# Kernel optimization log

Measured on AMD Instinct MI355X. Metric: run time of the kernel, lower is better.

The kernel has to match this reference:

```python
import jax, jax.numpy as jnp
import numpy as np

N_HEAD = 32
N_KV_HEAD = 8
HEAD_DIM = 64
ROPE_THETA = 10000.0


def apply_rope(x):
    # x: [B, H, T, D], interleaved-pair RoPE (rotary_embedding_torch style)
    B, H, T, D = x.shape
    inv_freq = 1.0 / (ROPE_THETA ** (jnp.arange(0, D, 2, dtype=jnp.float32) / D))  # [D/2]
    ang = jnp.arange(T, dtype=jnp.float32)[:, None] * inv_freq[None, :]  # [T, D/2]
    cos = jnp.cos(ang)[None, None].astype(x.dtype)  # [1,1,T,D/2]
    sin = jnp.sin(ang)[None, None].astype(x.dtype)
    xe = x[..., 0::2]
    xo = x[..., 1::2]
    re = xe * cos - xo * sin
    ro = xo * cos + xe * sin
    return jnp.stack([re, ro], axis=-1).reshape(B, H, T, D)


def setup_inputs() -> dict:
    key = jax.random.key(0)
    ks = jax.random.split(key, 5)
    B, T, C = 2, 2048, 2048
    kv_dim = N_KV_HEAD * HEAD_DIM
    s = 0.02
    return {
        "x": jax.random.normal(ks[0], (B, T, C), jnp.float32),
        "wq": jax.random.normal(ks[1], (C, C), jnp.float32) * s,
        "wk": jax.random.normal(ks[2], (C, kv_dim), jnp.float32) * s,
        "wv": jax.random.normal(ks[3], (C, kv_dim), jnp.float32) * s,
        "wo": jax.random.normal(ks[4], (C, C), jnp.float32) * s,
    }


def reference(x, wq, wk, wv, wo):
    B, T, C = x.shape
    hd = HEAD_DIM
    q = (x @ wq).reshape(B, T, N_HEAD, hd).transpose(0, 2, 1, 3)      # [B,H,T,d]
    k = (x @ wk).reshape(B, T, N_KV_HEAD, hd).transpose(0, 2, 1, 3)   # [B,Hkv,T,d]
    v = (x @ wv).reshape(B, T, N_KV_HEAD, hd).transpose(0, 2, 1, 3)
    q = apply_rope(q)
    k = apply_rope(k)
    rep = N_HEAD // N_KV_HEAD
    k = jnp.repeat(k, rep, axis=1)  # repeat_interleave over head dim
    v = jnp.repeat(v, rep, axis=1)
    att = jnp.einsum('bhqd,bhkd->bhqk', q, k) * (1.0 / np.sqrt(hd))
    causal = jnp.tril(jnp.ones((T, T), dtype=bool))
    att = jnp.where(causal[None, None], att, jnp.finfo(att.dtype).min)
    att = jax.nn.softmax(att, axis=-1)
    y = jnp.einsum('bhqk,bhkd->bhqd', att, v)
    y = y.transpose(0, 2, 1, 3).reshape(B, T, C)
    return y @ wo
```

## Files before the change

### kernel.cpp

```cpp
#include <hip/hip_runtime.h>
#include <hip/hip_bf16.h>
#include <cstdint>
#include <cstddef>


using bf16 = __hip_bfloat16;
using f32x4  = __attribute__((ext_vector_type(4))) float;
using f32x16 = __attribute__((ext_vector_type(16))) float;
using short8 = __attribute__((ext_vector_type(8))) short;
using u32x4  = __attribute__((ext_vector_type(4))) unsigned int;

typedef __attribute__((address_space(1))) const void* gp1_t;
typedef __attribute__((address_space(3))) void*       lp3_t;

#define GLOAD_LDS16(g, l)                                                     \
  __builtin_amdgcn_global_load_lds((gp1_t)(const void*)(g), (lp3_t)(void*)(l), 16, 0, 0)

#define MFMA32(a, b, c) __builtin_amdgcn_mfma_f32_32x32x16_bf16(a, b, c, 0, 0, 0)

static constexpr int Bd  = 2;
static constexpr int Td  = 2048;
static constexpr int Cd  = 2048;
static constexpr int NH  = 32;
static constexpr int NKV = 8;
static constexpr int HD  = 64;
static constexpr int Md  = Bd * Td;

__device__ inline float bf2f(unsigned short u) {
  union { unsigned int i; float f; } v; v.i = ((unsigned int)u) << 16; return v.f;
}
__device__ inline unsigned short f2bfbits(float f) {
  union { float f; unsigned int u; } v; v.f = f;
  unsigned int r = v.u + 0x7fffu + ((v.u >> 16) & 1u);
  return (unsigned short)(r >> 16);
}
__device__ inline unsigned int pkbf(float a, float b) {
  unsigned int r;
  asm("v_cvt_pk_bf16_f32 %0, %1, %2" : "=v"(r) : "v"(a), "v"(b));
  return r;
}
__device__ inline void plswapf(float& a, float& b) {
  asm("v_permlane32_swap_b32 %0, %1" : "+v"(a), "+v"(b));
}
__device__ inline void plswapu(unsigned int& a, unsigned int& b) {
  asm("v_permlane32_swap_b32 %0, %1" : "+v"(a), "+v"(b));
}
__device__ inline float hmax16(const f32x16& v) {
  float a0 = fmaxf(v[0], v[1]),   a1 = fmaxf(v[2], v[3]);
  float a2 = fmaxf(v[4], v[5]),   a3 = fmaxf(v[6], v[7]);
  float a4 = fmaxf(v[8], v[9]),   a5 = fmaxf(v[10], v[11]);
  float a6 = fmaxf(v[12], v[13]), a7 = fmaxf(v[14], v[15]);
  float b0 = fmaxf(a0, a1), b1 = fmaxf(a2, a3);
  float b2 = fmaxf(a4, a5), b3 = fmaxf(a6, a7);
  return fmaxf(fmaxf(b0, b1), fmaxf(b2, b3));
}
__device__ inline float hsum16(const f32x16& v) {
  float a0 = v[0]+v[1],   a1 = v[2]+v[3],   a2 = v[4]+v[5],   a3 = v[6]+v[7];
  float a4 = v[8]+v[9],   a5 = v[10]+v[11], a6 = v[12]+v[13], a7 = v[14]+v[15];
  float b0 = a0+a1, b1 = a2+a3, b2 = a4+a5, b3 = a6+a7;
  return (b0+b1)+(b2+b3);
}

__global__ __launch_bounds__(256) void prep1_kernel(const float* __restrict__ x,
                                                    const float* __restrict__ wq,
                                                    const float* __restrict__ wk,
                                                    const float* __restrict__ wv,
                                                    bf16* __restrict__ xb,
                                                    bf16* __restrict__ w1) {
  __shared__ float tile[32][33];
  int bid = blockIdx.x, tid = threadIdx.x;
  if (bid < 8192) {
    int i = bid * 256 + tid;
    float4 v = ((const float4*)x)[i];
    ushort4 o;
    o.x = f2bfbits(v.x); o.y = f2bfbits(v.y); o.z = f2bfbits(v.z); o.w = f2bfbits(v.w);
    ((ushort4*)xb)[i] = o;
    return;
  }
  const float* in; bf16* out; int Cc, bx, by;
  if (bid < 12288)      { int l = bid - 8192;  in = wq; out = w1;                        Cc = 2048; bx = l & 63; by = l >> 6; }
  else if (bid < 13312) { int l = bid - 12288; in = wk; out = w1 + (size_t)2048 * 2048;  Cc = 512;  bx = l & 15; by = l >> 4; }
  else                  { int l = bid - 13312; in = wv; out = w1 + (size_t)2560 * 2048;  Cc = 512;  bx = l & 15; by = l >> 4; }
  int tx = tid & 31, ty = tid >> 5;
  int col = bx * 32 + tx;
#pragma unroll
  for (int i = 0; i < 4; ++i) {
    int row = by * 32 + ty + i * 8;
    tile[ty + i * 8][tx] = in[(size_t)row * Cc + col];
  }
  __syncthreads();
#pragma unroll
  for (int i = 0; i < 4; ++i) {
    int orow = bx * 32 + ty + i * 8;
    int ocol = by * 32 + tx;
    out[(size_t)orow * 2048 + ocol] = __float2bfloat16(tile[tx][ty + i * 8]);
  }
}

__global__ __launch_bounds__(256) void transpose_f2b(const float* __restrict__ in,
                                                     bf16* __restrict__ out,
                                                     int R, int Cc) {
  __shared__ float tile[32][33];
  int tx = threadIdx.x & 31, ty = threadIdx.x >> 5;
  int bx = blockIdx.x, by = blockIdx.y;
  int col = bx * 32 + tx;
#pragma unroll
  for (int i = 0; i < 4; ++i) {
    int row = by * 32 + ty + i * 8;
    tile[ty + i * 8][tx] = in[(size_t)row * Cc + col];
  }
  __syncthreads();
#pragma unroll
  for (int i = 0; i < 4; ++i) {
    int orow = bx * 32 + ty + i * 8;
    int ocol = by * 32 + tx;
    out[(size_t)orow * R + ocol] = __float2bfloat16(tile[tx][ty + i * 8]);
  }
}

template <int MODE>
__global__ __launch_bounds__(256, 2) void gemm_bf16(const bf16* __restrict__ A,
                                                    const bf16* __restrict__ Bt,
                                                    void* __restrict__ Cp,
                                                    int M, int N, int K) {
  __shared__ __align__(16) bf16 Al[2][128 * 64];
  __shared__ __align__(16) bf16 Bl[2][128 * 64];
  int tid = threadIdx.x;
  int w = tid >> 6, lane = tid & 63;
  int lr = lane & 15, lg = lane >> 4;
  int m0 = blockIdx.x * 128, n0 = blockIdx.y * 128;
  int wr = w >> 1, wc = w & 1;
  f32x4 acc[4][4] = {};

  size_t Kb = (size_t)K * 2;
  int c8 = lane & 7, r8 = lane >> 3;
  const char* Asrc = (const char*)A + (size_t)(m0 + w * 8 + r8) * Kb + ((c8 ^ r8) << 4);
  const char* Bsrc = (const char*)Bt + (size_t)(n0 + w * 8 + r8) * Kb + ((c8 ^ r8) << 4);

#define GSTAGE(kt, bb) do {                                                   \
    char* ald = (char*)&Al[bb][0] + w * 1024;                                 \
    char* bld = (char*)&Bl[bb][0] + w * 1024;                                 \
    _Pragma("unroll")                                                         \
    for (int j = 0; j < 4; ++j) {                                             \
      GLOAD_LDS16(Asrc + (size_t)j * 32 * Kb + (size_t)(kt) * 2, ald + j * 4096); \
      GLOAD_LDS16(Bsrc + (size_t)j * 32 * Kb + (size_t)(kt) * 2, bld + j * 4096); \
    }                                                                         \
  } while (0)

  int nkt = K >> 6;
  GSTAGE(0, 0);
  __syncthreads();

  for (int t = 0; t < nkt; ++t) {
    int cur = t & 1;
    if (t + 1 < nkt) GSTAGE((t + 1) << 6, cur ^ 1);
    const char* Ab = (const char*)&Al[cur][0];
    const char* Bb = (const char*)&Bl[cur][0];
#pragma unroll
    for (int kk = 0; kk < 2; ++kk) {
      short8 af[4], bfr[4];
#pragma unroll
      for (int f = 0; f < 4; ++f) {
        int ra = wr * 64 + f * 16 + lr;
        int rb = wc * 64 + f * 16 + lr;
        int cb = (((kk << 2) | lg) ^ (lr & 7)) << 4;
        af[f]  = *(const short8*)(Ab + (size_t)ra * 128 + cb);
        bfr[f] = *(const short8*)(Bb + (size_t)rb * 128 + cb);
      }
#pragma unroll
      for (int i = 0; i < 4; ++i)
#pragma unroll
        for (int j = 0; j < 4; ++j)
          acc[i][j] = __builtin_amdgcn_mfma_f32_16x16x32_bf16(af[i], bfr[j], acc[i][j], 0, 0, 0);
    }
    __syncthreads();
  }
#undef GSTAGE

  bf16* Qb  = (bf16*)Cp;
  bf16* Kb2 = Qb + (size_t)Bd * NH * Td * HD;
  bf16* Vtb = Kb2 + (size_t)Bd * NKV * Td * HD;

  if (MODE == 3 && n0 >= 2560) {
    int h  = (n0 - 2560 + wc * 64) >> 6;
    int b  = m0 >> 11;
    int tg = (m0 & 2047) + wr * 64;
    char* tb = (w < 2 ? (char*)&Al[0][0] : (char*)&Bl[0][0]) + (w & 1) * 8192;
#pragma unroll
    for (int i = 0; i < 4; ++i)
#pragma unroll
      for (int j = 0; j < 4; ++j)
#pragma unroll
        for (int r = 0; r < 4; r += 2) {
          int d  = j * 16 + lr;
          int tt = i * 16 + lg * 4 + r;
          unsigned int pk = pkbf(acc[i][j][r], acc[i][j][r + 1]);
          *(unsigned int*)(tb + (((size_t)d * 128 + tt * 2) ^ ((d & 7) << 4))) = pk;
        }
    asm volatile("s_waitcnt lgkmcnt(0)" ::: "memory");
    __builtin_amdgcn_sched_barrier(0);
    char* Vdst = (char*)Vtb + ((((size_t)b * NKV + h) * 64) * Td + tg) * 2;
#pragma unroll
    for (int p = 0; p < 8; ++p) {
      int d  = p * 8 + (lane >> 3);
      int tc = lane & 7;
      u32x4 v = *(const u32x4*)(tb + (((size_t)d * 128 + tc * 16) ^ ((d & 7) << 4)));
      *(u32x4*)(Vdst + (size_t)d * Td * 2 + tc * 16) = v;
    }
    return;
  }

  if (MODE == 3) {
    const float RC = -0.41524101186092029f;
    float sc = (n0 < 2048) ? 0.18033688011112042f : 1.0f;
    int odd = lane & 1;
#pragma unroll
    for (int j = 0; j < 4; ++j) {
      int ncol = n0 + wc * 64 + j * 16 + lr;
      int d  = ncol & 63;
      float inv = __builtin_amdgcn_exp2f((float)(d >> 1) * RC);
#pragma unroll
      for (int i = 0; i < 4; ++i) {
#pragma unroll
        for (int r = 0; r < 4; ++r) {
          int mrow = m0 + wr * 64 + i * 16 + lg * 4 + r;
          int t = mrow & 2047;
          float v = acc[i][j][r];
          float p = __shfl_xor(v, 1);
          float rev = (float)t * inv * 0.15915494309189535f;
          rev = rev - floorf(rev);
          float s = __builtin_amdgcn_sinf(rev);
          float c = __builtin_amdgcn_cosf(rev);
          float res = odd ? (v * c + p * s) : (v * c - p * s);
          res *= sc;
          int b = mrow >> 11;
          if (n0 < 2048) {
            int h = ncol >> 6;
            Qb[(((size_t)b * NH + h) * Td + t) * HD + d] = __float2bfloat16(res);
          } else {
            int h = (ncol - 2048) >> 6;
            Kb2[(((size_t)b * NKV + h) * Td + t) * HD + d] = __float2bfloat16(res);
          }
        }
      }
    }
    return;
  }

#pragma unroll
  for (int i = 0; i < 4; ++i)
#pragma unroll
    for (int j = 0; j < 4; ++j)
#pragma unroll
      for (int r = 0; r < 4; ++r) {
        int mrow = m0 + wr * 64 + i * 16 + lg * 4 + r;
        int ncol = n0 + wc * 64 + j * 16 + lr;
        ((float*)Cp)[(size_t)mrow * N + ncol] = acc[i][j][r];
      }
}

__global__ __launch_bounds__(512, 4) void attn_kernel(const bf16* __restrict__ Q,
                                                      const bf16* __restrict__ K,
                                                      const bf16* __restrict__ Vt,
                                                      bf16* __restrict__ Y) {
  __shared__ __align__(16) char lds[2 * 16384];
  int tid = threadIdx.x, w = tid >> 6, lane = tid & 63;
  int lq = lane & 31;
  int H  = lane >> 5;
  int qb = 7 - (int)blockIdx.y;
  int bh = blockIdx.x;
  int b = bh >> 5, h = bh & 31, kvh = h >> 2;
  int q0w = qb * 256 + w * 32;
  int qg  = q0w + lq;
  int tmax = qb * 4 + (w >> 1);
  int Nt   = qb * 4 + 4;

  const bf16* Qp = Q + (((size_t)b * NH + h) * Td) * HD;
  const char* Kg = (const char*)(K + (((size_t)b * NKV + kvh) * Td) * HD);
  const char* Vg = (const char*)(Vt + (((size_t)b * NKV + kvh) * HD) * Td);

  short8 qf[4];
#pragma unroll
  for (int ck = 0; ck < 4; ++ck)
    qf[ck] = *(const short8*)(Qp + (size_t)qg * HD + ck * 16 + H * 8);

  int srow   = lane >> 3;
  int scol16 = ((lane & 7) ^ srow) << 4;
  const char* Ksrc0 = Kg + (size_t)(w * 8 + srow) * 128 + scol16;
  const char* Vsrc0 = Vg + (size_t)(w * 8 + srow) * 4096 + scol16;
  char* KldsW[2] = { lds + w * 1024,          lds + 16384 + w * 1024 };
  char* VldsW[2] = { lds + 8192 + w * 1024,   lds + 24576 + w * 1024 };

#define STAGE_KV(tt, bb) do {                                                 \
    GLOAD_LDS16(Ksrc0 + (size_t)(tt) * 64 * 128, KldsW[bb]);                  \
    GLOAD_LDS16(Vsrc0 + (size_t)(tt) * 128,      VldsW[bb]);                  \
  } while (0)

  f32x16 acc0 = {}, acc1 = {};
  float m = -3e38f, l = 0.0f;
  int swz = (lq & 7) << 4;
  int rb0 = lq * 128, rb1 = (32 + lq) * 128;

  STAGE_KV(0, 0);
  asm volatile("s_waitcnt vmcnt(0)" ::: "memory");
  __syncthreads();

  for (int t = 0; t < Nt; ++t) {
    int cur = t & 1;
    if (t + 1 < Nt) STAGE_KV(t + 1, cur ^ 1);
    if (t <= tmax) {
      const char* Kl = lds + cur * 16384;
      const char* Vl = Kl + 8192;
      f32x16 s0 = {}, s1 = {};
      __builtin_amdgcn_s_setprio(1);
#pragma unroll
      for (int ck = 0; ck < 4; ++ck) {
        int c = (H * 16 + ck * 32) ^ swz;
        short8 kf0 = *(const short8*)(Kl + rb0 + c);
        short8 kf1 = *(const short8*)(Kl + rb1 + c);
        s0 = MFMA32(kf0, qf[ck], s0);
        s1 = MFMA32(kf1, qf[ck], s1);
      }
      __builtin_amdgcn_s_setprio(0);
      if (t == tmax) {
        int kvb = t * 64;
#pragma unroll
        for (int rr = 0; rr < 16; ++rr) {
          int krel = (rr & 3) + 8 * (rr >> 2) + 4 * H;
          if (kvb + krel > qg)      s0[rr] = -3e38f;
          if (kvb + 32 + krel > qg) s1[rr] = -3e38f;
        }
      }
      float mx = fmaxf(hmax16(s0), hmax16(s1));
      {
        float mb = mx;
        asm("" : "+v"(mb));
        plswapf(mx, mb);
        mx = fmaxf(mx, mb);
      }
      if (__any(mx > m + 8.0f)) {
        float mn = fmaxf(m, mx);
        float al = __builtin_amdgcn_exp2f(m - mn);
        m = mn;
        l *= al;
#pragma unroll
        for (int rr = 0; rr < 16; ++rr) { acc0[rr] *= al; acc1[rr] *= al; }
      }
#pragma unroll
      for (int rr = 0; rr < 16; ++rr) {
        s0[rr] = __builtin_amdgcn_exp2f(s0[rr] - m);
        s1[rr] = __builtin_amdgcn_exp2f(s1[rr] - m);
      }
      float ps = hsum16(s0) + hsum16(s1);
      {
        float pb = ps;
        asm("" : "+v"(pb));
        plswapf(ps, pb);
        ps += pb;
      }
      l += ps;
      short8 pf[4];
#pragma unroll
      for (int tt = 0; tt < 2; ++tt) {
        const f32x16& sv = tt ? s1 : s0;
#pragma unroll
        for (int a2 = 0; a2 < 2; ++a2) {
          unsigned int A0 = pkbf(sv[8*a2 + 0], sv[8*a2 + 1]);
          unsigned int A1 = pkbf(sv[8*a2 + 2], sv[8*a2 + 3]);
          unsigned int B0 = pkbf(sv[8*a2 + 4], sv[8*a2 + 5]);
          unsigned int B1 = pkbf(sv[8*a2 + 6], sv[8*a2 + 7]);
          plswapu(A0, B0);
          plswapu(A1, B1);
          u32x4 t4;
          t4[0] = A0; t4[1] = A1; t4[2] = B0; t4[3] = B1;
          pf[2*tt + a2] = __builtin_bit_cast(short8, t4);
        }
      }
      __builtin_amdgcn_s_setprio(1);
#pragma unroll
      for (int ks = 0; ks < 4; ++ks) {
        int c = (H * 16 + ks * 32) ^ swz;
        short8 vf0 = *(const short8*)(Vl + rb0 + c);
        short8 vf1 = *(const short8*)(Vl + rb1 + c);
        acc0 = MFMA32(vf0, pf[ks], acc0);
        acc1 = MFMA32(vf1, pf[ks], acc1);
      }
      __builtin_amdgcn_s_setprio(0);
    }
    asm volatile("s_waitcnt vmcnt(0)" ::: "memory");
    __syncthreads();
  }
#undef STAGE_KV

  float rn = 1.0f / l;
  bf16* Yp = Y + ((size_t)b * Td + qg) * Cd + h * HD;
#pragma unroll
  for (int rr = 0; rr < 16; rr += 2) {
    int d = (rr & 3) + 8 * (rr >> 2) + 4 * H;
    unsigned int w0 = pkbf(acc0[rr] * rn, acc0[rr + 1] * rn);
    unsigned int w1 = pkbf(acc1[rr] * rn, acc1[rr + 1] * rn);
    *(unsigned int*)(Yp + d)      = w0;
    *(unsigned int*)(Yp + 32 + d) = w1;
  }
}

extern "C" void kernel_launch(void* const* d_in, const int* in_sizes, int n_in,
                              void* d_out, int out_size, void* d_ws, size_t ws_size,
                              hipStream_t stream) {
  const float* x  = (const float*)d_in[0];
  const float* wq = (const float*)d_in[1];
  const float* wk = (const float*)d_in[2];
  const float* wv = (const float*)d_in[3];
  const float* wo = (const float*)d_in[4];

  char* ws = (char*)d_ws;
  const size_t o_xb = 0;
  const size_t o_w1 = o_xb + (size_t)Md * Cd * 2;
  const size_t o_Q  = o_w1 + (size_t)3072 * Cd * 2;
  const size_t o_K  = o_Q + (size_t)Bd * NH * Td * HD * 2;
  const size_t o_V  = o_K + (size_t)Bd * NKV * Td * HD * 2;

  bf16* xb  = (bf16*)(ws + o_xb);
  bf16* w1  = (bf16*)(ws + o_w1);
  bf16* Qb  = (bf16*)(ws + o_Q);
  bf16* Kb  = (bf16*)(ws + o_K);
  bf16* Vtb = (bf16*)(ws + o_V);
  bf16* yb  = xb;

  prep1_kernel<<<dim3(14336), dim3(256), 0, stream>>>(x, wq, wk, wv, xb, w1);
  gemm_bf16<3><<<dim3(Md / 128, 3072 / 128), dim3(256), 0, stream>>>(xb, w1, Qb, Md, 3072, Cd);
  transpose_f2b<<<dim3(Cd / 32, Cd / 32), dim3(256), 0, stream>>>(wo, w1, Cd, Cd);
  attn_kernel<<<dim3(Bd * NH, 8), dim3(512), 0, stream>>>(Qb, Kb, Vtb, yb);
  gemm_bf16<2><<<dim3(Md / 128, Cd / 128), dim3(256), 0, stream>>>(yb, w1, d_out, Md, Cd, Cd);
}
```

Measured before the change: 198.3 us.

## Use two waves per GEMM block with 64x128 per-wave tiles

Restructures the bf16 GEMM from four waves each owning a 64x64 sub-tile to two waves each owning 64 rows by the full 128 columns. This doubles accumulators per wave and raises register-level reuse of B fragments, cutting LDS reads per MFMA. It also rewrites staging, the V-transpose epilogue and the RoPE epilogue for the new layout. The trade-off is fewer waves per block for latency hiding and more register pressure, which may lower occupancy.

```diff
diff --git a/kernel.cpp b/kernel.cpp
--- a/kernel.cpp
+++ b/kernel.cpp
@@ -119,7 +119,7 @@
 }
 
 template <int MODE>
-__global__ __launch_bounds__(256, 2) void gemm_bf16(const bf16* __restrict__ A,
+__global__ __launch_bounds__(128, 2) void gemm_bf16(const bf16* __restrict__ A,
                                                     const bf16* __restrict__ Bt,
                                                     void* __restrict__ Cp,
                                                     int M, int N, int K) {
@@ -129,21 +129,20 @@
   int w = tid >> 6, lane = tid & 63;
   int lr = lane & 15, lg = lane >> 4;
   int m0 = blockIdx.x * 128, n0 = blockIdx.y * 128;
-  int wr = w >> 1, wc = w & 1;
-  f32x4 acc[4][4] = {};
+  f32x4 acc[4][8] = {};
 
   size_t Kb = (size_t)K * 2;
   int c8 = lane & 7, r8 = lane >> 3;
-  const char* Asrc = (const char*)A + (size_t)(m0 + w * 8 + r8) * Kb + ((c8 ^ r8) << 4);
-  const char* Bsrc = (const char*)Bt + (size_t)(n0 + w * 8 + r8) * Kb + ((c8 ^ r8) << 4);
+  const char* Asrc = (const char*)A + (size_t)(m0 + w * 64 + r8) * Kb + ((c8 ^ r8) << 4);
+  const char* Bsrc = (const char*)Bt + (size_t)(n0 + w * 64 + r8) * Kb + ((c8 ^ r8) << 4);
 
 #define GSTAGE(kt, bb) do {                                                   \
-    char* ald = (char*)&Al[bb][0] + w * 1024;                                 \
-    char* bld = (char*)&Bl[bb][0] + w * 1024;                                 \
+    char* ald = (char*)&Al[bb][0] + w * 8192;                                 \
+    char* bld = (char*)&Bl[bb][0] + w * 8192;                                 \
     _Pragma("unroll")                                                         \
-    for (int j = 0; j < 4; ++j) {                                             \
-      GLOAD_LDS16(Asrc + (size_t)j * 32 * Kb + (size_t)(kt) * 2, ald + j * 4096); \
-      GLOAD_LDS16(Bsrc + (size_t)j * 32 * Kb + (size_t)(kt) * 2, bld + j * 4096); \
+    for (int j = 0; j < 8; ++j) {                                             \
+      GLOAD_LDS16(Asrc + (size_t)j * 8 * Kb + (size_t)(kt) * 2, ald + j * 1024); \
+      GLOAD_LDS16(Bsrc + (size_t)j * 8 * Kb + (size_t)(kt) * 2, bld + j * 1024); \
     }                                                                         \
   } while (0)
 
@@ -158,19 +157,18 @@
     const char* Bb = (const char*)&Bl[cur][0];
 #pragma unroll
     for (int kk = 0; kk < 2; ++kk) {
-      short8 af[4], bfr[4];
-#pragma unroll
-      for (int f = 0; f < 4; ++f) {
-        int ra = wr * 64 + f * 16 + lr;
-        int rb = wc * 64 + f * 16 + lr;
-        int cb = (((kk << 2) | lg) ^ (lr & 7)) << 4;
-        af[f]  = *(const short8*)(Ab + (size_t)ra * 128 + cb);
-        bfr[f] = *(const short8*)(Bb + (size_t)rb * 128 + cb);
-      }
+      int cb = (((kk << 2) | lg) ^ (lr & 7)) << 4;
+      short8 af[4], bfr[8];
+#pragma unroll
+      for (int f = 0; f < 4; ++f)
+        af[f] = *(const short8*)(Ab + (size_t)(w * 64 + f * 16 + lr) * 128 + cb);
+#pragma unroll
+      for (int j = 0; j < 8; ++j)
+        bfr[j] = *(const short8*)(Bb + (size_t)(j * 16 + lr) * 128 + cb);
 #pragma unroll
       for (int i = 0; i < 4; ++i)
 #pragma unroll
-        for (int j = 0; j < 4; ++j)
+        for (int j = 0; j < 8; ++j)
           acc[i][j] = __builtin_amdgcn_mfma_f32_16x16x32_bf16(af[i], bfr[j], acc[i][j], 0, 0, 0);
     }
     __syncthreads();
@@ -182,14 +180,14 @@
   bf16* Vtb = Kb2 + (size_t)Bd * NKV * Td * HD;
 
   if (MODE == 3 && n0 >= 2560) {
-    int h  = (n0 - 2560 + wc * 64) >> 6;
     int b  = m0 >> 11;
-    int tg = (m0 & 2047) + wr * 64;
-    char* tb = (w < 2 ? (char*)&Al[0][0] : (char*)&Bl[0][0]) + (w & 1) * 8192;
+    int tg = (m0 & 2047) + w * 64;
+    int h0 = (n0 - 2560) >> 6;
+    char* tb = (char*)&Al[0][0] + w * 16384;
 #pragma unroll
     for (int i = 0; i < 4; ++i)
 #pragma unroll
-      for (int j = 0; j < 4; ++j)
+      for (int j = 0; j < 8; ++j)
 #pragma unroll
         for (int r = 0; r < 4; r += 2) {
           int d  = j * 16 + lr;
@@ -199,13 +197,14 @@
         }
     asm volatile("s_waitcnt lgkmcnt(0)" ::: "memory");
     __builtin_amdgcn_sched_barrier(0);
-    char* Vdst = (char*)Vtb + ((((size_t)b * NKV + h) * 64) * Td + tg) * 2;
-#pragma unroll
-    for (int p = 0; p < 8; ++p) {
+    char* Vdst = (char*)Vtb + ((((size_t)b * NKV + h0) * 64) * Td + tg) * 2;
+#pragma unroll
+    for (int p = 0; p < 16; ++p) {
       int d  = p * 8 + (lane >> 3);
       int tc = lane & 7;
       u32x4 v = *(const u32x4*)(tb + (((size_t)d * 128 + tc * 16) ^ ((d & 7) << 4)));
-      *(u32x4*)(Vdst + (size_t)d * Td * 2 + tc * 16) = v;
+      int hh = d >> 6, dd = d & 63;
+      *(u32x4*)(Vdst + ((size_t)hh * 64 + dd) * Td * 2 + tc * 16) = v;
     }
     return;
   }
@@ -215,15 +214,15 @@
     float sc = (n0 < 2048) ? 0.18033688011112042f : 1.0f;
     int odd = lane & 1;
 #pragma unroll
-    for (int j = 0; j < 4; ++j) {
-      int ncol = n0 + wc * 64 + j * 16 + lr;
+    for (int j = 0; j < 8; ++j) {
+      int ncol = n0 + j * 16 + lr;
       int d  = ncol & 63;
       float inv = __builtin_amdgcn_exp2f((float)(d >> 1) * RC);
 #pragma unroll
       for (int i = 0; i < 4; ++i) {
 #pragma unroll
         for (int r = 0; r < 4; ++r) {
-          int mrow = m0 + wr * 64 + i * 16 + lg * 4 + r;
+          int mrow = m0 + w * 64 + i * 16 + lg * 4 + r;
           int t = mrow & 2047;
           float v = acc[i][j][r];
           float p = __shfl_xor(v, 1);
@@ -250,11 +249,11 @@
 #pragma unroll
   for (int i = 0; i < 4; ++i)
 #pragma unroll
-    for (int j = 0; j < 4; ++j)
+    for (int j = 0; j < 8; ++j)
 #pragma unroll
       for (int r = 0; r < 4; ++r) {
-        int mrow = m0 + wr * 64 + i * 16 + lg * 4 + r;
-        int ncol = n0 + wc * 64 + j * 16 + lr;
+        int mrow = m0 + w * 64 + i * 16 + lg * 4 + r;
+        int ncol = n0 + j * 16 + lr;
         ((float*)Cp)[(size_t)mrow * N + ncol] = acc[i][j][r];
       }
 }
@@ -428,8 +427,8 @@
   bf16* yb  = xb;
 
   prep1_kernel<<<dim3(14336), dim3(256), 0, stream>>>(x, wq, wk, wv, xb, w1);
-  gemm_bf16<3><<<dim3(Md / 128, 3072 / 128), dim3(256), 0, stream>>>(xb, w1, Qb, Md, 3072, Cd);
+  gemm_bf16<3><<<dim3(Md / 128, 3072 / 128), dim3(128), 0, stream>>>(xb, w1, Qb, Md, 3072, Cd);
   transpose_f2b<<<dim3(Cd / 32, Cd / 32), dim3(256), 0, stream>>>(wo, w1, Cd, Cd);
   attn_kernel<<<dim3(Bd * NH, 8), dim3(512), 0, stream>>>(Qb, Kb, Vtb, yb);
-  gemm_bf16<2><<<dim3(Md / 128, Cd / 128), dim3(256), 0, stream>>>(yb, w1, d_out, Md, Cd, Cd);
-}
+  gemm_bf16<2><<<dim3(Md / 128, Cd / 128), dim3(128), 0, stream>>>(yb, w1, d_out, Md, Cd, Cd);
+}
```

Result: slower. 227.7 us (+14.8%).
